# Optimization experiments

Measured on AMD Instinct MI355X. Metric: run time of the kernel, lower is better.

## Reference

```python
import math
import jax, jax.numpy as jnp
import numpy as np

B, S, D, H = 2, 2048, 2048, 16
HD = D // H  # head_dim = 128


def setup_inputs() -> dict:
    key = jax.random.key(0)
    ks = jax.random.split(key, 5)
    x = jax.random.normal(ks[0], (B, S, D), dtype=jnp.float32)
    # torch nn.Linear weights are [out_features, in_features]
    wq = jax.random.normal(ks[1], (D, D), dtype=jnp.float32) * 0.02
    wk = jax.random.normal(ks[2], (D, D), dtype=jnp.float32) * 0.02
    wv = jax.random.normal(ks[3], (D, D), dtype=jnp.float32) * 0.02
    wo = jax.random.normal(ks[4], (D, D), dtype=jnp.float32) * 0.02
    # llama-style rotary frequencies: freq_cis[t, i] = exp(1j * t / 10000^(2i/hd))
    inv_freq = 1.0 / (10000.0 ** (jnp.arange(0, HD, 2, dtype=jnp.float32) / HD))  # [HD/2]
    angles = jnp.arange(S, dtype=jnp.float32)[:, None] * inv_freq[None, :]  # [S, HD/2]
    freq_cos = jnp.cos(angles)
    freq_sin = jnp.sin(angles)
    # additive causal mask (0 on/below diagonal, large negative above)
    mask = jnp.triu(jnp.full((S, S), -1e9, dtype=jnp.float32), k=1)
    return {"x": x, "wq": wq, "wk": wk, "wv": wv, "wo": wo,
            "freq_cos": freq_cos, "freq_sin": freq_sin, "mask": mask}


def _rope(t, cos, sin):
    # t: [B, H, S, HD]; cos/sin: [S, HD/2]. Consecutive pairs form complex numbers.
    b, h, s, hd = t.shape
    tr = t.reshape(b, h, s, hd // 2, 2)
    re, im = tr[..., 0], tr[..., 1]
    c = cos[None, None, :, :]
    sn = sin[None, None, :, :]
    out_re = re * c - im * sn
    out_im = re * sn + im * c
    return jnp.stack([out_re, out_im], axis=-1).reshape(b, h, s, hd)


def reference(x, wq, wk, wv, wo, freq_cos, freq_sin, mask):
    b, s, d = x.shape
    hd = 2 * freq_cos.shape[-1]
    h = wq.shape[0] // hd
    # projections (torch Linear: y = x @ W.T)
    q = jnp.einsum('bsd,ed->bse', x, wq).reshape(b, s, h, hd).transpose(0, 2, 1, 3)
    k = jnp.einsum('bsd,ed->bse', x, wk).reshape(b, s, h, hd).transpose(0, 2, 1, 3)
    v = jnp.einsum('bsd,ed->bse', x, wv).reshape(b, s, h, hd).transpose(0, 2, 1, 3)
    q = _rope(q, freq_cos, freq_sin)
    k = _rope(k, freq_cos, freq_sin)
    scores = jnp.einsum('bhqd,bhkd->bhqk', q, k) / math.sqrt(hd)  # [B,H,S,S]
    scores = scores + mask[None, None, :, :]
    attn = jax.nn.softmax(scores, axis=-1)
    o = jnp.einsum('bhqk,bhkd->bhqd', attn, v)
    o = o.transpose(0, 2, 1, 3).reshape(b, s, h * hd)
    return jnp.einsum('bse,de->bsd', o, wo)
```

## Files before the change

### kernel.cpp

```cpp
#include <hip/hip_runtime.h>
#include <stdint.h>

#define BB  2
#define SS  2048
#define DD  2048
#define HH  16
#define HDD 128
#define MM  (BB * SS)

typedef __attribute__((ext_vector_type(8)))  short short8;
typedef __attribute__((ext_vector_type(4)))  float f32x4;
typedef __attribute__((ext_vector_type(16))) float f32x16;
typedef unsigned int   u32;
typedef unsigned short u16;
typedef __attribute__((ext_vector_type(4))) u16 u16x4;
typedef __attribute__((ext_vector_type(2))) u32 u32x2;
typedef __attribute__((ext_vector_type(4))) u32 u32x4;

static __device__ __forceinline__ u16 f2bf(float f) {
  u32 u = __builtin_bit_cast(u32, f);
  u32 r = u + 0x7fffu + ((u >> 16) & 1u);
  return (u16)(r >> 16);
}

static __device__ __forceinline__ u32 cvtpk(float a, float b) {
  u32 r;
  asm("v_cvt_pk_bf16_f32 %0, %1, %2" : "=v"(r) : "v"(a), "v"(b));
  return r;
}
static __device__ __forceinline__ void permswap(u32& a, u32& b) {
  asm volatile("v_permlane32_swap_b32 %0, %1" : "+v"(a), "+v"(b));
}

__global__ void cvt_all(const float* __restrict__ x,  const float* __restrict__ wq,
                        const float* __restrict__ wk, const float* __restrict__ wv,
                        const float* __restrict__ wo,
                        u16* __restrict__ xb, u16* __restrict__ wqkv,
                        u16* __restrict__ wob) {
  const int NX = (MM * DD) / 4;
  const int NW = (DD * DD) / 4;
  int i = blockIdx.x * blockDim.x + threadIdx.x;
  const float* s; u16* d; int off;
  if (i < NX) { s = x; d = xb; off = i; }
  else {
    int j = i - NX; int w = j >> 20; off = j & (NW - 1);
    s = (w == 0) ? wq : (w == 1) ? wk : (w == 2) ? wv : wo;
    d = (w < 3) ? (wqkv + (size_t)w * DD * DD) : wob;
  }
  f32x4 v = *(const f32x4*)(s + (size_t)off * 4);
  u16x4 o;
#pragma unroll
  for (int j = 0; j < 4; ++j) o[j] = f2bf(v[j]);
  *(u16x4*)(d + (size_t)off * 4) = o;
}

template <int MODE>
__global__ __launch_bounds__(256) void gemm2(const u16* __restrict__ A,
                                             const u16* __restrict__ Bw,
                                             u16* __restrict__ Cq,
                                             u16* __restrict__ Ck,
                                             u16* __restrict__ Cvt,
                                             float* __restrict__ Cf,
                                             int M, int N, int K,
                                             const float* __restrict__ fc,
                                             const float* __restrict__ fs) {
  __shared__ __align__(16) u16 Al[3][128 * 32];
  __shared__ __align__(16) u16 Bl[3][128 * 32];
  const int tid  = threadIdx.x;
  const int wave = tid >> 6, lane = tid & 63;
  const int m0 = blockIdx.y * 128, n0 = blockIdx.x * 128;
  const int wr = (wave >> 1) * 64, wc = (wave & 1) * 64;
  const int lrow = lane & 15, lk = (lane >> 4) * 8;

  f32x4 acc[4][4] = {};

#define GSTAGE(T, BUF)                                                                  \
  {                                                                                     \
    int koff = (T) * 32;                                                                \
    _Pragma("unroll")                                                                   \
    for (int i_ = 0; i_ < 2; ++i_) {                                                    \
      int idx = tid + i_ * 256;                                                         \
      int row = idx >> 2, kc = (idx & 3) * 8;                                           \
      const u16* ga = A  + (size_t)(m0 + row) * K + koff + kc;                          \
      const u16* gb = Bw + (size_t)(n0 + row) * K + koff + kc;                          \
      __builtin_amdgcn_global_load_lds((const __attribute__((address_space(1))) u32*)ga,\
                                       (__attribute__((address_space(3))) u32*)(&Al[BUF][0] + idx * 8), \
                                       16, 0, 0);                                       \
      __builtin_amdgcn_global_load_lds((const __attribute__((address_space(1))) u32*)gb,\
                                       (__attribute__((address_space(3))) u32*)(&Bl[BUF][0] + idx * 8), \
                                       16, 0, 0);                                       \
    }                                                                                   \
  }

  const int NT = K / 32;
  GSTAGE(0, 0);
  int cur = 0;
  for (int t = 0; t < NT; ++t) {
    int nxt = cur + 1; if (nxt == 3) nxt = 0;
    if (t + 1 < NT) {
      GSTAGE(t + 1, nxt);
      asm volatile("s_waitcnt vmcnt(4)" ::: "memory");
    } else {
      asm volatile("s_waitcnt vmcnt(0)" ::: "memory");
    }
    __syncthreads();

    const u16* Ab = &Al[cur][0];
    const u16* Bb = &Bl[cur][0];
    short8 af[4], bfr[4];
#pragma unroll
    for (int tt = 0; tt < 4; ++tt) {
      af[tt]  = *(const short8*)(Ab + (wr + tt * 16 + lrow) * 32 + lk);
      bfr[tt] = *(const short8*)(Bb + (wc + tt * 16 + lrow) * 32 + lk);
    }
#pragma unroll
    for (int mt = 0; mt < 4; ++mt)
#pragma unroll
      for (int nt = 0; nt < 4; ++nt)
        acc[mt][nt] = __builtin_amdgcn_mfma_f32_16x16x32_bf16(af[mt], bfr[nt], acc[mt][nt], 0, 0, 0);
    cur = nxt;
  }
#undef GSTAGE

  const int dr = (lane >> 4) * 4;
  if constexpr (MODE == 1) {
#pragma unroll
    for (int mt = 0; mt < 4; ++mt)
#pragma unroll
      for (int nt = 0; nt < 4; ++nt)
#pragma unroll
        for (int i = 0; i < 4; ++i) {
          size_t r = (size_t)(m0 + wr + mt * 16 + dr + i);
          size_t c = (size_t)(n0 + wc + nt * 16 + lrow);
          Cf[r * N + c] = acc[mt][nt][i];
        }
  } else {
    const int region = n0 >> 11;
    if (region < 2) {
      u16* Cd = region ? Ck : Cq;
#pragma unroll
      for (int mt = 0; mt < 4; ++mt)
#pragma unroll
        for (int nt = 0; nt < 4; ++nt) {
          int c  = n0 + wc + nt * 16 + lrow;
          int cl = c & 2047;
          int dh = cl & 127, pi = dh >> 1;
          float sgn = (dh & 1) ? 1.f : -1.f;
#pragma unroll
          for (int i = 0; i < 4; ++i) {
            int r  = m0 + wr + mt * 16 + dr + i;
            int s_ = r & (SS - 1);
            float v  = acc[mt][nt][i];
            float pv = __shfl_xor(v, 1, 64);
            Cd[(size_t)r * 2048 + cl] = f2bf(v * fc[s_ * 64 + pi] + pv * (sgn * fs[s_ * 64 + pi]));
          }
        }
    } else {
#pragma unroll
      for (int mt = 0; mt < 4; ++mt)
#pragma unroll
        for (int nt = 0; nt < 4; ++nt) {
          int cl = (n0 - 4096) + wc + nt * 16 + lrow;
          int rr = m0 + wr + mt * 16 + dr;
          int b  = rr >> 11, s0 = rr & 2047;
          u16x4 pk;
#pragma unroll
          for (int i = 0; i < 4; ++i) pk[i] = f2bf(acc[mt][nt][i]);
          *(u16x4*)(Cvt + ((size_t)b * 2048 + cl) * 2048 + s0) = pk;
        }
    }
  }
}

__global__ __launch_bounds__(256, 2) void attn_kernel(const u16* __restrict__ Q,
                                                      const u16* __restrict__ K,
                                                      const u16* __restrict__ Vt,
                                                      u16* __restrict__ O) {
  __shared__ __align__(16) u16 Kl[2][64 * 128];
  __shared__ __align__(16) u16 Vl[2][128 * 64];

  const int tid = threadIdx.x, wave = tid >> 6, lane = tid & 63;
  const int l31 = lane & 31, hi = lane >> 5;
  const int bh = blockIdx.x, b = bh >> 4, h = bh & 15;
  const int y = blockIdx.y;
  const int qt = (y < 8) ? y : (23 - y);
  const size_t base    = ((size_t)b * SS) * DD + (size_t)h * HDD;
  const size_t vt_base = (size_t)bh * HDD * SS;
  const int swz = (l31 & 7) << 4;

#define STAGE(KT, BUF)                                                              \
  {                                                                                 \
    int k0s = (KT) * 64;                                                            \
    _Pragma("unroll")                                                               \
    for (int i_ = 0; i_ < 4; ++i_) {                                                \
      int idx = tid + i_ * 256;                                                     \
      int kr = idx >> 4, c_ = idx & 15;                                             \
      const u16* gk = K + base + (size_t)(k0s + kr) * DD + ((c_ ^ (kr & 7)) * 8);   \
      __builtin_amdgcn_global_load_lds((const __attribute__((address_space(1))) u32*)gk, \
                                       (__attribute__((address_space(3))) u32*)(&Kl[BUF][0] + idx * 8), \
                                       16, 0, 0);                                   \
      int dv = idx >> 3, c2 = idx & 7;                                              \
      const u16* gv = Vt + vt_base + (size_t)dv * SS + k0s + ((c2 ^ (dv & 7)) * 8); \
      __builtin_amdgcn_global_load_lds((const __attribute__((address_space(1))) u32*)gv, \
                                       (__attribute__((address_space(3))) u32*)(&Vl[BUF][0] + idx * 8), \
                                       16, 0, 0);                                   \
    }                                                                               \
  }

  const int qw = qt * 128 + wave * 32;
  const int q_ = qw + l31;

  short8 qf[8];
#pragma unroll
  for (int kc = 0; kc < 8; ++kc)
    qf[kc] = *(const short8*)(Q + base + (size_t)(qw + l31) * DD + kc * 16 + hi * 8);

  f32x16 oacc[4] = {};
  float m_i = -1e30f, l_p = 0.f;

  int buf = 0;
  STAGE(0, 0);

  const int ntiles = 2 * qt + 2;
  for (int kt = 0; kt < ntiles; ++kt) {
    const int k0 = kt * 64;
    if (kt + 1 < ntiles) {
      STAGE(kt + 1, buf ^ 1);
      asm volatile("s_waitcnt vmcnt(8)" ::: "memory");
    } else {
      asm volatile("s_waitcnt vmcnt(0)" ::: "memory");
    }
    __syncthreads();

    if (k0 <= qw + 31) {
      const u16* Kb_ = &Kl[buf][0];
      const u16* Vb_ = &Vl[buf][0];

      f32x16 st[2] = {};
      __builtin_amdgcn_s_setprio(1);
#pragma unroll
      for (int kc = 0; kc < 8; ++kc) {
        int by0 = (l31 * 256)        + ((kc * 32 + hi * 16) ^ swz);
        int by1 = ((32 + l31) * 256) + ((kc * 32 + hi * 16) ^ swz);
        short8 a0 = *(const short8*)(Kb_ + (by0 >> 1));
        short8 a1 = *(const short8*)(Kb_ + (by1 >> 1));
        st[0] = __builtin_amdgcn_mfma_f32_32x32x16_bf16(a0, qf[kc], st[0], 0, 0, 0);
        st[1] = __builtin_amdgcn_mfma_f32_32x32x16_bf16(a1, qf[kc], st[1], 0, 0, 0);
      }
      __builtin_amdgcn_s_setprio(0);

      const float scale2 = 0.08838834764831845f * 1.44269504088896340736f;
      float mx = -1e30f;
#pragma unroll
      for (int kb = 0; kb < 2; ++kb)
#pragma unroll
        for (int r = 0; r < 16; ++r) {
          float s = st[kb][r] * scale2;
          int key = k0 + kb * 32 + (r & 3) + ((r >> 2) << 3) + (hi << 2);
          if (key > q_) s = -1e30f;
          st[kb][r] = s;
          mx = fmaxf(mx, s);
        }
      mx = fmaxf(mx, __shfl_xor(mx, 32, 64));

      if (__any(mx > m_i + 8.f)) {
        float mn  = fmaxf(m_i, mx);
        float esc = exp2f(m_i - mn);
        m_i = mn; l_p *= esc;
#pragma unroll
        for (int db = 0; db < 4; ++db)
#pragma unroll
          for (int r = 0; r < 16; ++r) oacc[db][r] *= esc;
      }
      float sum = 0.f;
#pragma unroll
      for (int kb = 0; kb < 2; ++kb)
#pragma unroll
        for (int r = 0; r < 16; ++r) {
          float e = exp2f(st[kb][r] - m_i);
          st[kb][r] = e;
          sum += e;
        }
      l_p += sum;

      __builtin_amdgcn_s_setprio(1);
#pragma unroll
      for (int kb = 0; kb < 2; ++kb) {
#pragma unroll
        for (int half = 0; half < 2; ++half) {
          const int rb = half * 8;
          u32 w0 = cvtpk(st[kb][rb + 0], st[kb][rb + 1]);
          u32 w1 = cvtpk(st[kb][rb + 2], st[kb][rb + 3]);
          u32 w2 = cvtpk(st[kb][rb + 4], st[kb][rb + 5]);
          u32 w3 = cvtpk(st[kb][rb + 6], st[kb][rb + 7]);
          permswap(w0, w2);
          permswap(w1, w3);
          short8 pf = __builtin_bit_cast(short8, (u32x4){w0, w1, w2, w3});
          const int ktv = kb * 2 + half;
#pragma unroll
          for (int db = 0; db < 4; ++db) {
            int d = db * 32 + l31;
            int by = d * 128 + ((ktv * 32 + hi * 16) ^ swz);
            short8 vf = *(const short8*)(Vb_ + (by >> 1));
            oacc[db] = __builtin_amdgcn_mfma_f32_32x32x16_bf16(vf, pf, oacc[db], 0, 0, 0);
          }
        }
      }
      __builtin_amdgcn_s_setprio(0);
    }
    __syncthreads();
    buf ^= 1;
  }

  float lt  = l_p + __shfl_xor(l_p, 32, 64);
  float inv = 1.f / lt;
#pragma unroll
  for (int db = 0; db < 4; ++db)
#pragma unroll
    for (int g = 0; g < 4; ++g) {
      int d0 = db * 32 + 8 * g + 4 * hi;
      u32x2 pk;
      pk[0] = cvtpk(oacc[db][4 * g + 0] * inv, oacc[db][4 * g + 1] * inv);
      pk[1] = cvtpk(oacc[db][4 * g + 2] * inv, oacc[db][4 * g + 3] * inv);
      *(u32x2*)(O + base + (size_t)q_ * DD + d0) = pk;
    }
#undef STAGE
}

extern "C" void kernel_launch(void* const* d_in, const int* in_sizes, int n_in,
                              void* d_out, int out_size, void* d_ws, size_t ws_size,
                              hipStream_t stream) {
  (void)in_sizes; (void)n_in; (void)out_size; (void)ws_size;
  const float* x  = (const float*)d_in[0];
  const float* wq = (const float*)d_in[1];
  const float* wk = (const float*)d_in[2];
  const float* wv = (const float*)d_in[3];
  const float* wo = (const float*)d_in[4];
  const float* fc = (const float*)d_in[5];
  const float* fs = (const float*)d_in[6];
  float* out = (float*)d_out;

  const size_t XBUF = (size_t)MM * DD * 2;
  const size_t WBUF = (size_t)DD * DD * 2;
  char* ws = (char*)d_ws;
  u16* xb   = (u16*)(ws);
  u16* Qb   = (u16*)(ws + XBUF);
  u16* Kb   = (u16*)(ws + 2 * XBUF);
  u16* Vtb  = (u16*)(ws + 3 * XBUF);
  u16* wqkv = (u16*)(ws + 4 * XBUF);
  u16* wob  = (u16*)(ws + 4 * XBUF + 3 * WBUF);
  u16* Ob   = xb;

  const int ncv = (MM * DD) / 4 + 4 * ((DD * DD) / 4);
  cvt_all<<<ncv / 256, 256, 0, stream>>>(x, wq, wk, wv, wo, xb, wqkv, wob);

  gemm2<4><<<dim3(48, 32), 256, 0, stream>>>(xb, wqkv, Qb, Kb, Vtb, nullptr,
                                             MM, 3 * DD, DD, fc, fs);

  attn_kernel<<<dim3(32, 16), 256, 0, stream>>>(Qb, Kb, Vtb, Ob);

  gemm2<1><<<dim3(16, 32), 256, 0, stream>>>(Ob, wob, nullptr, nullptr, nullptr, out,
                                             MM, DD, DD, nullptr, nullptr);
}
```

Measured before the change: 275.8 us.

## Replace QKV projection GEMM with 256x256-tile, 8-wave direct-to-LDS pipelined kernel

The fused QKV projection moves from a 128x128 tile, 4-wave GEMM to a 256x256 tile, 8-wave kernel. It streams A/B tiles with global_load_lds into XOR-swizzled LDS, double-buffers them, and interleaves quarter-tile loads with MFMA sub-blocks under s_setprio and explicit waitcnt/barriers. The aim is higher operand reuse, fewer bank conflicts, and load latency hidden behind MFMA work. The cost is 128KB of LDS per block, a large accumulator register footprint, only 384 blocks, and many barriers per K step. The output GEMM is split out unchanged as its own kernel.

```diff
diff --git a/kernel.cpp b/kernel.cpp
--- a/kernel.cpp
+++ b/kernel.cpp
@@ -54,16 +54,161 @@
   *(u16x4*)(d + (size_t)off * 4) = o;
 }
 
-template <int MODE>
-__global__ __launch_bounds__(256) void gemm2(const u16* __restrict__ A,
-                                             const u16* __restrict__ Bw,
-                                             u16* __restrict__ Cq,
-                                             u16* __restrict__ Ck,
-                                             u16* __restrict__ Cvt,
-                                             float* __restrict__ Cf,
-                                             int M, int N, int K,
-                                             const float* __restrict__ fc,
-                                             const float* __restrict__ fs) {
+__global__ __launch_bounds__(512, 2) void gemm8_qkv(const u16* __restrict__ A,
+                                                    const u16* __restrict__ Bw,
+                                                    u16* __restrict__ Cq,
+                                                    u16* __restrict__ Ck,
+                                                    u16* __restrict__ Cvt,
+                                                    const float* __restrict__ fc,
+                                                    const float* __restrict__ fs) {
+  const int K = DD;
+  __shared__ __align__(16) u16 Al[2][256 * 64];
+  __shared__ __align__(16) u16 Bl[2][256 * 64];
+  const int tid = threadIdx.x;
+  const int wid = tid >> 6, lane = tid & 63;
+  const int wm = wid >> 2, wn = wid & 3;
+  const int m0b = blockIdx.y * 256, n0b = blockIdx.x * 256;
+  const int lrow = lane & 15, kh = lane >> 4;
+  const int s8 = lrow & 7;
+
+  f32x4 acc[8][4] = {};
+  short8 ar[4][2], br[2][2];
+
+#define STG8(Tt, BUF, HT) do {                                                        \
+    int k0s = (Tt) * 64;                                                              \
+    _Pragma("unroll")                                                                 \
+    for (int j_ = 0; j_ < 2; ++j_) {                                                  \
+      int i_ = tid + j_ * 512;                                                        \
+      int rl_ = i_ >> 3, c_ = i_ & 7;                                                 \
+      int sc_ = c_ ^ (rl_ & 7);                                                       \
+      const u16* g_ = (((HT) & 1) ? Bw : A)                                           \
+          + (size_t)((((HT) & 1) ? n0b : m0b) + ((HT) >> 1) * 128 + rl_) * K          \
+          + k0s + sc_ * 8;                                                            \
+      u16* l_ = (((HT) & 1) ? &Bl[BUF][0] : &Al[BUF][0]) + ((HT) >> 1) * 8192 + i_ * 8; \
+      __builtin_amdgcn_global_load_lds((const __attribute__((address_space(1))) u32*)g_, \
+                                       (__attribute__((address_space(3))) u32*)l_,    \
+                                       16, 0, 0);                                     \
+    } } while (0)
+
+#define RD_A(MH)                                                                      \
+    _Pragma("unroll")                                                                 \
+    for (int f = 0; f < 4; ++f)                                                       \
+      _Pragma("unroll")                                                               \
+      for (int ks = 0; ks < 2; ++ks)                                                  \
+        ar[f][ks] = *(const short8*)(Ab + ((MH) * 64 + f * 16 + lrow) * 64            \
+                                        + ((ks * 4 + kh) ^ s8) * 8);
+
+#define RD_B(NH)                                                                      \
+    _Pragma("unroll")                                                                 \
+    for (int g = 0; g < 2; ++g)                                                       \
+      _Pragma("unroll")                                                               \
+      for (int ks = 0; ks < 2; ++ks)                                                  \
+        br[g][ks] = *(const short8*)(Bb + ((wn & 1) * 64 + (NH) * 32 + g * 16 + lrow) * 64 \
+                                        + ((ks * 4 + kh) ^ s8) * 8);
+
+#define WAIT_LGKM()                                                                   \
+    asm volatile("s_waitcnt lgkmcnt(0)" ::: "memory");                                \
+    __builtin_amdgcn_sched_barrier(0);
+
+#define MM16(MH, NH)                                                                  \
+    __builtin_amdgcn_s_setprio(1);                                                    \
+    _Pragma("unroll")                                                                 \
+    for (int f = 0; f < 4; ++f)                                                       \
+      _Pragma("unroll")                                                               \
+      for (int g = 0; g < 2; ++g)                                                     \
+        _Pragma("unroll")                                                             \
+        for (int ks = 0; ks < 2; ++ks)                                                \
+          acc[(MH) * 4 + f][(NH) * 2 + g] = __builtin_amdgcn_mfma_f32_16x16x32_bf16(  \
+              ar[f][ks], br[g][ks], acc[(MH) * 4 + f][(NH) * 2 + g], 0, 0, 0);        \
+    __builtin_amdgcn_s_setprio(0);
+
+  STG8(0, 0, 0); STG8(0, 0, 1); STG8(0, 0, 2); STG8(0, 0, 3);
+
+  const int NT = K / 64;
+  for (int t = 0; t < NT; ++t) {
+    const int bt = t & 1;
+    const u16* Ab = &Al[bt][0] + wm * 8192;
+    const u16* Bb = &Bl[bt][0] + (wn >> 1) * 8192;
+    const bool more = (t + 1 < NT);
+
+    if (more) { STG8(t + 1, bt ^ 1, 0); asm volatile("s_waitcnt vmcnt(2)" ::: "memory"); }
+    else      {                         asm volatile("s_waitcnt vmcnt(0)" ::: "memory"); }
+    __builtin_amdgcn_s_barrier();
+
+    RD_A(0); RD_B(0);
+    if (more) STG8(t + 1, bt ^ 1, 1);
+    __builtin_amdgcn_s_barrier();
+    WAIT_LGKM();
+    MM16(0, 0);
+    __builtin_amdgcn_s_barrier();
+
+    RD_A(1);
+    if (more) STG8(t + 1, bt ^ 1, 2);
+    __builtin_amdgcn_s_barrier();
+    WAIT_LGKM();
+    MM16(1, 0);
+    __builtin_amdgcn_s_barrier();
+
+    RD_B(1);
+    if (more) STG8(t + 1, bt ^ 1, 3);
+    __builtin_amdgcn_s_barrier();
+    WAIT_LGKM();
+    MM16(1, 1);
+    __builtin_amdgcn_s_barrier();
+
+    RD_A(0);
+    __builtin_amdgcn_s_barrier();
+    WAIT_LGKM();
+    MM16(0, 1);
+    __builtin_amdgcn_s_barrier();
+  }
+#undef STG8
+#undef RD_A
+#undef RD_B
+#undef WAIT_LGKM
+#undef MM16
+
+  const int dr = kh * 4;
+  const int region = n0b >> 11;
+  if (region < 2) {
+    u16* Cd = region ? Ck : Cq;
+#pragma unroll
+    for (int mf = 0; mf < 8; ++mf)
+#pragma unroll
+      for (int nf = 0; nf < 4; ++nf) {
+        int c  = n0b + wn * 64 + nf * 16 + lrow;
+        int cl = c & 2047;
+        int dh = cl & 127, pi = dh >> 1;
+        float sgn = (dh & 1) ? 1.f : -1.f;
+#pragma unroll
+        for (int i = 0; i < 4; ++i) {
+          int r  = m0b + wm * 128 + mf * 16 + dr + i;
+          int s_ = r & (SS - 1);
+          float v  = acc[mf][nf][i];
+          float pv = __shfl_xor(v, 1, 64);
+          Cd[(size_t)r * 2048 + cl] = f2bf(v * fc[s_ * 64 + pi] + pv * (sgn * fs[s_ * 64 + pi]));
+        }
+      }
+  } else {
+#pragma unroll
+    for (int mf = 0; mf < 8; ++mf)
+#pragma unroll
+      for (int nf = 0; nf < 4; ++nf) {
+        int cl = (n0b - 4096) + wn * 64 + nf * 16 + lrow;
+        int rr = m0b + wm * 128 + mf * 16 + dr;
+        int b  = rr >> 11, s0 = rr & 2047;
+        u16x4 pk;
+#pragma unroll
+        for (int i = 0; i < 4; ++i) pk[i] = f2bf(acc[mf][nf][i]);
+        *(u16x4*)(Cvt + ((size_t)b * 2048 + cl) * 2048 + s0) = pk;
+      }
+  }
+}
+
+__global__ __launch_bounds__(256) void gemm_o(const u16* __restrict__ A,
+                                              const u16* __restrict__ Bw,
+                                              float* __restrict__ Cf,
+                                              int M, int N, int K) {
   __shared__ __align__(16) u16 Al[3][128 * 32];
   __shared__ __align__(16) u16 Bl[3][128 * 32];
   const int tid  = threadIdx.x;
@@ -123,53 +268,16 @@
 #undef GSTAGE
 
   const int dr = (lane >> 4) * 4;
-  if constexpr (MODE == 1) {
-#pragma unroll
-    for (int mt = 0; mt < 4; ++mt)
-#pragma unroll
-      for (int nt = 0; nt < 4; ++nt)
-#pragma unroll
-        for (int i = 0; i < 4; ++i) {
-          size_t r = (size_t)(m0 + wr + mt * 16 + dr + i);
-          size_t c = (size_t)(n0 + wc + nt * 16 + lrow);
-          Cf[r * N + c] = acc[mt][nt][i];
-        }
-  } else {
-    const int region = n0 >> 11;
-    if (region < 2) {
-      u16* Cd = region ? Ck : Cq;
-#pragma unroll
-      for (int mt = 0; mt < 4; ++mt)
-#pragma unroll
-        for (int nt = 0; nt < 4; ++nt) {
-          int c  = n0 + wc + nt * 16 + lrow;
-          int cl = c & 2047;
-          int dh = cl & 127, pi = dh >> 1;
-          float sgn = (dh & 1) ? 1.f : -1.f;
-#pragma unroll
-          for (int i = 0; i < 4; ++i) {
-            int r  = m0 + wr + mt * 16 + dr + i;
-            int s_ = r & (SS - 1);
-            float v  = acc[mt][nt][i];
-            float pv = __shfl_xor(v, 1, 64);
-            Cd[(size_t)r * 2048 + cl] = f2bf(v * fc[s_ * 64 + pi] + pv * (sgn * fs[s_ * 64 + pi]));
-          }
-        }
-    } else {
-#pragma unroll
-      for (int mt = 0; mt < 4; ++mt)
-#pragma unroll
-        for (int nt = 0; nt < 4; ++nt) {
-          int cl = (n0 - 4096) + wc + nt * 16 + lrow;
-          int rr = m0 + wr + mt * 16 + dr;
-          int b  = rr >> 11, s0 = rr & 2047;
-          u16x4 pk;
-#pragma unroll
-          for (int i = 0; i < 4; ++i) pk[i] = f2bf(acc[mt][nt][i]);
-          *(u16x4*)(Cvt + ((size_t)b * 2048 + cl) * 2048 + s0) = pk;
-        }
-    }
-  }
+#pragma unroll
+  for (int mt = 0; mt < 4; ++mt)
+#pragma unroll
+    for (int nt = 0; nt < 4; ++nt)
+#pragma unroll
+      for (int i = 0; i < 4; ++i) {
+        size_t r = (size_t)(m0 + wr + mt * 16 + dr + i);
+        size_t c = (size_t)(n0 + wc + nt * 16 + lrow);
+        Cf[r * N + c] = acc[mt][nt][i];
+      }
 }
 
 __global__ __launch_bounds__(256, 2) void attn_kernel(const u16* __restrict__ Q,
@@ -354,11 +462,9 @@
   const int ncv = (MM * DD) / 4 + 4 * ((DD * DD) / 4);
   cvt_all<<<ncv / 256, 256, 0, stream>>>(x, wq, wk, wv, wo, xb, wqkv, wob);
 
-  gemm2<4><<<dim3(48, 32), 256, 0, stream>>>(xb, wqkv, Qb, Kb, Vtb, nullptr,
-                                             MM, 3 * DD, DD, fc, fs);
+  gemm8_qkv<<<dim3(24, 16), 512, 0, stream>>>(xb, wqkv, Qb, Kb, Vtb, fc, fs);
 
   attn_kernel<<<dim3(32, 16), 256, 0, stream>>>(Qb, Kb, Vtb, Ob);
 
-  gemm2<1><<<dim3(16, 32), 256, 0, stream>>>(Ob, wob, nullptr, nullptr, nullptr, out,
-                                             MM, DD, DD, nullptr, nullptr);
-}
+  gemm_o<<<dim3(16, 32), 256, 0, stream>>>(Ob, wob, out, MM, DD, DD);
+}
```

After: 289.7 us. 1.05x slower.
